# Performance work log

Hardware: AMD Instinct MI355X
Metric: run time of the kernel (lower is better)

## Reference

```python
import jax, jax.numpy as jnp
import numpy as np

BATCH, VOCAB = 256, 50257

def setup_inputs() -> dict:
    key = jax.random.key(0)
    k1, k2 = jax.random.split(key)
    logits = jax.random.normal(k1, (BATCH, VOCAB), dtype=jnp.float32) * 4.0  # LM-like logit spread
    temperature = jax.random.uniform(k2, (), dtype=jnp.float32, minval=0.5, maxval=1.5)
    return {"logits": logits, "temperature": temperature, "top_k": 50}


def reference(logits, temperature, top_k):
    # temperature scale (dividing by 1.0 is identical to the torch skip-branch)
    scaled = logits / temperature
    # top-k mask: keep exactly the k selected positions, -inf elsewhere
    top_vals, top_idx = jax.lax.top_k(scaled, top_k)          # [B, k]
    b = jnp.arange(scaled.shape[0])[:, None]                  # [B, 1]
    masked = jnp.full_like(scaled, -jnp.inf).at[b, top_idx].set(top_vals)
    # softmax + multinomial(num_samples=1) == categorical over masked logits
    key = jax.random.key(42)
    sampled = jax.random.categorical(key, masked, axis=-1)    # [B]
    return sampled
```

## Files before the change

kernel.cpp:

```cpp
#include <hip/hip_runtime.h>
#include <stdint.h>


#define VOCAB 50257
#define BATCH 256
#define NT 1024
#define NBINS 4096
#define CAND_CAP 2048
#define FILTER_VAL 4.0f
#define SPEC_VAL 10.0f

__device__ __forceinline__ uint32_t rotl32(uint32_t v, int r) {
  return (v << r) | (v >> (32 - r));
}

__device__ __forceinline__ void threefry2x32_42(uint32_t& x0, uint32_t& x1) {
  const uint32_t ks0 = 0u;
  const uint32_t ks1 = 42u;
  const uint32_t ks2 = ks0 ^ ks1 ^ 0x1BD11BDAu;
  x0 += ks0; x1 += ks1;
#define TF_R(r) { x0 += x1; x1 = rotl32(x1, (r)); x1 ^= x0; }
  TF_R(13) TF_R(15) TF_R(26) TF_R(6)
  x0 += ks1; x1 += ks2 + 1u;
  TF_R(17) TF_R(29) TF_R(16) TF_R(24)
  x0 += ks2; x1 += ks0 + 2u;
  TF_R(13) TF_R(15) TF_R(26) TF_R(6)
  x0 += ks0; x1 += ks1 + 3u;
  TF_R(17) TF_R(29) TF_R(16) TF_R(24)
  x0 += ks1; x1 += ks2 + 4u;
  TF_R(13) TF_R(15) TF_R(26) TF_R(6)
  x0 += ks2; x1 += ks0 + 5u;
#undef TF_R
}

__device__ __forceinline__ float gumbel_at(uint32_t flat) {
  uint32_t x0 = 0u, x1 = flat;
  threefry2x32_42(x0, x1);
  uint32_t bits = x0 ^ x1;
  uint32_t fb = (bits >> 9) | 0x3f800000u;
  float f = __uint_as_float(fb) - 1.0f;
  float u = fmaxf(f, 1.17549435e-38f);
  float t = (float)log((double)u);
  float g = (float)(-log((double)(-t)));
  return g;
}

__device__ __forceinline__ uint32_t fkey(float x) {
  uint32_t u = __float_as_uint(x);
  return (u & 0x80000000u) ? ~u : (u | 0x80000000u);
}

extern "C" __global__ void __launch_bounds__(NT)
topk_sample_kernel(const float* __restrict__ logits,
                   const float* __restrict__ temp_p,
                   const int* __restrict__ topk_p,
                   int* __restrict__ out) {
  const int row = blockIdx.x;
  const int tid = threadIdx.x;
  const float temp = temp_p[0];
  const int K = topk_p[0];
  const float* rowp = logits + (size_t)row * VOCAB;

  const int pc = (4 - (row & 3)) & 3;
  const int nv4 = (VOCAB - pc) >> 2;
  const int tailbase = pc + (nv4 << 2);
  const int tailc = VOCAB - tailbase;
  const float4* body = (const float4*)(rowp + pc);

  __shared__ unsigned hist[NBINS];
  __shared__ unsigned wtot[16];
  __shared__ unsigned aboveWave[16];
  __shared__ int sh_tb, sh_total, sh_cnt, sh_ok;
  __shared__ unsigned ckey[CAND_CAP];
  __shared__ int cidx[CAND_CAP];
  __shared__ float wbv[16];
  __shared__ int wbi[16];

  const int lane = tid & 63;
  const int wave = tid >> 6;

  float bestv = -__builtin_huge_valf();
  int besti = 0x7fffffff;
  bool done = false;

  if (tid == 0) { sh_cnt = 0; sh_ok = 0; }
  __syncthreads();
  if (tid < pc) {
    if (rowp[tid] >= SPEC_VAL) {
      int p = atomicAdd(&sh_cnt, 1);
      if (p < CAND_CAP) cidx[p] = tid;
    }
  }
  int v = tid;
  for (; v + 3 * NT < nv4; v += 4 * NT) {
    float4 x0 = body[v];
    float4 x1 = body[v + NT];
    float4 x2 = body[v + 2 * NT];
    float4 x3 = body[v + 3 * NT];
#define PROC4(VX, b)                                                             \
    {                                                                            \
      int base_ = (b);                                                           \
      if (VX.x >= SPEC_VAL) { int p = atomicAdd(&sh_cnt, 1); if (p < CAND_CAP) cidx[p] = base_; }     \
      if (VX.y >= SPEC_VAL) { int p = atomicAdd(&sh_cnt, 1); if (p < CAND_CAP) cidx[p] = base_ + 1; } \
      if (VX.z >= SPEC_VAL) { int p = atomicAdd(&sh_cnt, 1); if (p < CAND_CAP) cidx[p] = base_ + 2; } \
      if (VX.w >= SPEC_VAL) { int p = atomicAdd(&sh_cnt, 1); if (p < CAND_CAP) cidx[p] = base_ + 3; } \
    }
    PROC4(x0, pc + (v << 2))
    PROC4(x1, pc + ((v + NT) << 2))
    PROC4(x2, pc + ((v + 2 * NT) << 2))
    PROC4(x3, pc + ((v + 3 * NT) << 2))
  }
  for (; v < nv4; v += NT) {
    float4 x = body[v];
    PROC4(x, pc + (v << 2))
  }
#undef PROC4
  if (tid < tailc) {
    if (rowp[tailbase + tid] >= SPEC_VAL) {
      int p = atomicAdd(&sh_cnt, 1);
      if (p < CAND_CAP) cidx[p] = tailbase + tid;
    }
  }
  __syncthreads();
  const int total = sh_cnt;

  if (total >= K && total <= CAND_CAP) {
    const int C = total;
    float s_mine = 0.0f;
    if (tid < C) {
      s_mine = rowp[cidx[tid]] / temp;
      ckey[tid] = fkey(s_mine);
    }
    __syncthreads();
    if (tid < C) {
      const uint32_t mk = ckey[tid];
      const int mi = cidx[tid];
      int rank = 0;
      for (int j = 0; j < C; ++j) {
        uint32_t k = ckey[j];
        rank += (k > mk || (k == mk && cidx[j] < mi)) ? 1 : 0;
      }
      if (rank == K - 1) {
        sh_ok = (mk > fkey(SPEC_VAL / temp)) ? 1 : 0;
      }
      if (rank < K) {
        float v2 = s_mine + gumbel_at((uint32_t)row * (uint32_t)VOCAB + (uint32_t)mi);
        bestv = v2; besti = mi;
      }
    }
    __syncthreads();
    if (sh_ok) {
      done = true;
    } else {
      bestv = -__builtin_huge_valf();
      besti = 0x7fffffff;
    }
  }

  if (!done) {
    uint32_t filt = fkey(FILTER_VAL);
    int tb = 0;
    for (;;) {
      for (int b = tid; b < NBINS; b += NT) hist[b] = 0u;
      __syncthreads();
      if (tid < pc) {
        uint32_t k = fkey(rowp[tid]);
        if (k >= filt) atomicAdd(&hist[k >> 20], 1u);
      }
      for (int w = tid; w < nv4; w += NT) {
        float4 x = body[w];
        uint32_t k0 = fkey(x.x), k1 = fkey(x.y), k2 = fkey(x.z), k3 = fkey(x.w);
        if (k0 >= filt) atomicAdd(&hist[k0 >> 20], 1u);
        if (k1 >= filt) atomicAdd(&hist[k1 >> 20], 1u);
        if (k2 >= filt) atomicAdd(&hist[k2 >> 20], 1u);
        if (k3 >= filt) atomicAdd(&hist[k3 >> 20], 1u);
      }
      if (tid < tailc) {
        uint32_t k = fkey(rowp[tailbase + tid]);
        if (k >= filt) atomicAdd(&hist[k >> 20], 1u);
      }
      __syncthreads();

      unsigned p = hist[4 * tid] + hist[4 * tid + 1] + hist[4 * tid + 2] + hist[4 * tid + 3];
      unsigned vv = p;
      for (int off = 1; off < 64; off <<= 1) {
        unsigned o = (unsigned)__shfl_down((int)vv, off);
        if (lane + off < 64) vv += o;
      }
      if (lane == 0) wtot[wave] = vv;
      __syncthreads();
      if (tid == 0) {
        unsigned acc = 0;
        for (int w = 15; w >= 0; --w) { aboveWave[w] = acc; acc += wtot[w]; }
        sh_total = (int)acc;
      }
      __syncthreads();
      unsigned above = aboveWave[wave] + (vv - p);
      if (above < (unsigned)K && above + p >= (unsigned)K) {
        int need = K - (int)above;
        for (int b = 3; b >= 0; --b) {
          unsigned c = hist[4 * tid + b];
          if (c >= (unsigned)need) { sh_tb = 4 * tid + b; break; }
          need -= (int)c;
        }
      }
      __syncthreads();
      if (sh_total >= K) { tb = sh_tb; break; }
      filt = 0u;
      __syncthreads();
    }

    const uint32_t cutk = (uint32_t)max(tb - 1, 0) << 20;
    if (tid == 0) sh_cnt = 0;
    __syncthreads();
    if (tid < pc) {
      if (fkey(rowp[tid]) >= cutk) {
        int p = atomicAdd(&sh_cnt, 1);
        if (p < CAND_CAP) cidx[p] = tid;
      }
    }
    for (int w = tid; w < nv4; w += NT) {
      float4 x = body[w];
      int base = pc + (w << 2);
      if (fkey(x.x) >= cutk) { int p = atomicAdd(&sh_cnt, 1); if (p < CAND_CAP) cidx[p] = base; }
      if (fkey(x.y) >= cutk) { int p = atomicAdd(&sh_cnt, 1); if (p < CAND_CAP) cidx[p] = base + 1; }
      if (fkey(x.z) >= cutk) { int p = atomicAdd(&sh_cnt, 1); if (p < CAND_CAP) cidx[p] = base + 2; }
      if (fkey(x.w) >= cutk) { int p = atomicAdd(&sh_cnt, 1); if (p < CAND_CAP) cidx[p] = base + 3; }
    }
    if (tid < tailc) {
      if (fkey(rowp[tailbase + tid]) >= cutk) {
        int p = atomicAdd(&sh_cnt, 1);
        if (p < CAND_CAP) cidx[p] = tailbase + tid;
      }
    }
    __syncthreads();
    const int C = min(sh_cnt, CAND_CAP);

    if (tid < C) {
      int idx = cidx[tid];
      float s = rowp[idx] / temp;
      ckey[tid] = fkey(s);
    }
    __syncthreads();

    if (tid < C) {
      const uint32_t mk = ckey[tid];
      const int mi = cidx[tid];
      int rank = 0;
      for (int j = 0; j < C; ++j) {
        uint32_t k = ckey[j];
        rank += (k > mk || (k == mk && cidx[j] < mi)) ? 1 : 0;
      }
      if (rank < K) {
        float s = rowp[mi] / temp;
        float v2 = s + gumbel_at((uint32_t)row * (uint32_t)VOCAB + (uint32_t)mi);
        bestv = v2; besti = mi;
      }
    }
    __syncthreads();
  }

  for (int off = 32; off > 0; off >>= 1) {
    float v2 = __shfl_down(bestv, off);
    int i2 = __shfl_down(besti, off);
    if (v2 > bestv || (v2 == bestv && i2 < besti)) { bestv = v2; besti = i2; }
  }
  if (lane == 0) { wbv[wave] = bestv; wbi[wave] = besti; }
  __syncthreads();
  if (tid == 0) {
    float bv = wbv[0];
    int bi = wbi[0];
    for (int w = 1; w < 16; ++w) {
      float v2 = wbv[w];
      int i2 = wbi[w];
      if (v2 > bv || (v2 == bv && i2 < bi)) { bv = v2; bi = i2; }
    }
    out[row] = bi;
  }
}

extern "C" void kernel_launch(void* const* d_in, const int* in_sizes, int n_in,
                              void* d_out, int out_size, void* d_ws, size_t ws_size,
                              hipStream_t stream) {
  const float* logits = (const float*)d_in[0];
  const float* temp_p = (const float*)d_in[1];
  const int* topk_p = (const int*)d_in[2];
  int* out = (int*)d_out;
  hipLaunchKernelGGL(topk_sample_kernel, dim3(BATCH), dim3(NT), 0, stream,
                     logits, temp_p, topk_p, out);
}
```

Before: 114.5 us.

## Split row filtering across segment blocks and add separate refine/fallback kernels

The single kernel, which used one 1024-thread block per row, becomes three kernels. A filter kernel runs 16 segment blocks per row, each collecting indices of logits at or above the speculative threshold into a per-segment workspace slot. A refine kernel gathers the segments, ranks the candidates, samples with Gumbel noise, and sets a per-row flag. A fallback kernel, which exits early for flagged rows, runs the histogram path for the rest. This spreads the bandwidth-bound scan over many more blocks and CUs, but adds two extra kernel launches, workspace traffic, and a per-segment cap of 64 candidates that sends overflowing rows to the fallback path.

```diff
diff --git a/kernel.cpp b/kernel.cpp
--- a/kernel.cpp
+++ b/kernel.cpp
@@ -5,6 +5,10 @@
 #define VOCAB 50257
 #define BATCH 256
 #define NT 1024
+#define NTF 256
+#define NSEG 16
+#define SEG4 786
+#define CAP_SEG 64
 #define NBINS 4096
 #define CAND_CAP 2048
 #define FILTER_VAL 4.0f
@@ -50,15 +54,14 @@
   return (u & 0x80000000u) ? ~u : (u | 0x80000000u);
 }
 
-extern "C" __global__ void __launch_bounds__(NT)
-topk_sample_kernel(const float* __restrict__ logits,
-                   const float* __restrict__ temp_p,
-                   const int* __restrict__ topk_p,
-                   int* __restrict__ out) {
-  const int row = blockIdx.x;
+extern "C" __global__ void __launch_bounds__(NTF)
+filter_kernel(const float* __restrict__ logits,
+              int* __restrict__ cnt,
+              int* __restrict__ cand) {
+  const int b = blockIdx.x;
+  const int row = b >> 4;
+  const int seg = b & 15;
   const int tid = threadIdx.x;
-  const float temp = temp_p[0];
-  const int K = topk_p[0];
   const float* rowp = logits + (size_t)row * VOCAB;
 
   const int pc = (4 - (row & 3)) & 3;
@@ -67,10 +70,153 @@
   const int tailc = VOCAB - tailbase;
   const float4* body = (const float4*)(rowp + pc);
 
+  __shared__ int lcnt;
+  if (tid == 0) lcnt = 0;
+  __syncthreads();
+
+  int* myc = cand + (b << 6);
+  const int st = seg * SEG4;
+  const int en = min(nv4, st + SEG4);
+  for (int v = st + tid; v < en; v += NTF) {
+    float4 x = body[v];
+    int base = pc + (v << 2);
+    if (x.x >= SPEC_VAL) { int p = atomicAdd(&lcnt, 1); if (p < CAP_SEG) myc[p] = base; }
+    if (x.y >= SPEC_VAL) { int p = atomicAdd(&lcnt, 1); if (p < CAP_SEG) myc[p] = base + 1; }
+    if (x.z >= SPEC_VAL) { int p = atomicAdd(&lcnt, 1); if (p < CAP_SEG) myc[p] = base + 2; }
+    if (x.w >= SPEC_VAL) { int p = atomicAdd(&lcnt, 1); if (p < CAP_SEG) myc[p] = base + 3; }
+  }
+  if (seg == 0 && tid < pc) {
+    if (rowp[tid] >= SPEC_VAL) { int p = atomicAdd(&lcnt, 1); if (p < CAP_SEG) myc[p] = tid; }
+  }
+  if (seg == NSEG - 1 && tid < tailc) {
+    if (rowp[tailbase + tid] >= SPEC_VAL) {
+      int p = atomicAdd(&lcnt, 1); if (p < CAP_SEG) myc[p] = tailbase + tid;
+    }
+  }
+  __syncthreads();
+  if (tid == 0) cnt[b] = lcnt;
+}
+
+extern "C" __global__ void __launch_bounds__(NTF)
+refine_kernel(const float* __restrict__ logits,
+              const float* __restrict__ temp_p,
+              const int* __restrict__ topk_p,
+              int* __restrict__ out,
+              const int* __restrict__ cnt,
+              const int* __restrict__ cand,
+              int* __restrict__ flags) {
+  const int row = blockIdx.x;
+  const int tid = threadIdx.x;
+  const int lane = tid & 63;
+  const int wave = tid >> 6;
+
+  __shared__ int scnt[NSEG], soff[NSEG];
+  __shared__ int sh_total, sh_ok;
+  __shared__ unsigned ckey[CAND_CAP];
+  __shared__ int cidx[CAND_CAP];
+  __shared__ float wbv[4];
+  __shared__ int wbi[4];
+
+  if (tid < NSEG) scnt[tid] = cnt[(row << 4) + tid];
+  if (tid == 0) sh_ok = 0;
+  __syncthreads();
+  if (tid == 0) {
+    int acc = 0; int ovf = 0;
+    for (int s = 0; s < NSEG; ++s) {
+      soff[s] = acc;
+      if (scnt[s] > CAP_SEG) ovf = 1;
+      acc += scnt[s];
+    }
+    sh_total = ovf ? -1 : acc;
+  }
+  __syncthreads();
+  const int total = sh_total;
+  const int K = topk_p[0];
+  const float temp = temp_p[0];
+
+  const bool ok_path = (total >= K && total <= CAND_CAP);
+  if (ok_path) {
+    {
+      int s = tid >> 4, j0 = tid & 15;
+      const int* src = cand + (((row << 4) + s) << 6);
+      for (int j = j0; j < scnt[s]; j += 16) cidx[soff[s] + j] = src[j];
+    }
+    __syncthreads();
+    const float* rowp = logits + (size_t)row * VOCAB;
+    for (int c = tid; c < total; c += NTF) {
+      ckey[c] = fkey(rowp[cidx[c]] / temp);
+    }
+    __syncthreads();
+
+    float bestv = -__builtin_huge_valf();
+    int besti = 0x7fffffff;
+    const uint32_t cutkey = fkey(SPEC_VAL / temp);
+    for (int c = tid; c < total; c += NTF) {
+      const uint32_t mk = ckey[c];
+      const int mi = cidx[c];
+      int rank = 0;
+      for (int j = 0; j < total; ++j) {
+        uint32_t k = ckey[j];
+        rank += (k > mk || (k == mk && cidx[j] < mi)) ? 1 : 0;
+      }
+      if (rank == K - 1) {
+        sh_ok = (mk > cutkey) ? 1 : 0;
+      }
+      if (rank < K) {
+        float s = rowp[mi] / temp;
+        float v = s + gumbel_at((uint32_t)row * (uint32_t)VOCAB + (uint32_t)mi);
+        if (v > bestv || (v == bestv && mi < besti)) { bestv = v; besti = mi; }
+      }
+    }
+    __syncthreads();
+    if (sh_ok) {
+      for (int off = 32; off > 0; off >>= 1) {
+        float v2 = __shfl_down(bestv, off);
+        int i2 = __shfl_down(besti, off);
+        if (v2 > bestv || (v2 == bestv && i2 < besti)) { bestv = v2; besti = i2; }
+      }
+      if (lane == 0) { wbv[wave] = bestv; wbi[wave] = besti; }
+      __syncthreads();
+      if (tid == 0) {
+        float bv = wbv[0]; int bi = wbi[0];
+        for (int w = 1; w < 4; ++w) {
+          if (wbv[w] > bv || (wbv[w] == bv && wbi[w] < bi)) { bv = wbv[w]; bi = wbi[w]; }
+        }
+        out[row] = bi;
+        flags[row] = 1;
+      }
+    } else if (tid == 0) {
+      flags[row] = 0;
+    }
+  } else if (tid == 0) {
+    flags[row] = 0;
+  }
+}
+
+extern "C" __global__ void __launch_bounds__(NT)
+fallback_kernel(const float* __restrict__ logits,
+                const float* __restrict__ temp_p,
+                const int* __restrict__ topk_p,
+                int* __restrict__ out,
+                const int* __restrict__ flags) {
+  const int row = blockIdx.x;
+  if (flags[row]) return;
+
+  const int tid = threadIdx.x;
+  const float temp = temp_p[0];
+  const int K = topk_p[0];
+  const float* rowp = logits + (size_t)row * VOCAB;
+
+  const int pc = (4 - (row & 3)) & 3;
+  const int nv4 = (VOCAB - pc) >> 2;
+  const int tailbase = pc + (nv4 << 2);
+  const int tailc = VOCAB - tailbase;
+  const float4* body = (const float4*)(rowp + pc);
+
   __shared__ unsigned hist[NBINS];
   __shared__ unsigned wtot[16];
   __shared__ unsigned aboveWave[16];
-  __shared__ int sh_tb, sh_total, sh_cnt, sh_ok;
+  __shared__ int sh_tb, sh_total, sh_cnt;
   __shared__ unsigned ckey[CAND_CAP];
   __shared__ int cidx[CAND_CAP];
   __shared__ float wbv[16];
@@ -81,184 +227,107 @@
 
   float bestv = -__builtin_huge_valf();
   int besti = 0x7fffffff;
-  bool done = false;
-
-  if (tid == 0) { sh_cnt = 0; sh_ok = 0; }
+
+  uint32_t filt = fkey(FILTER_VAL);
+  int tb = 0;
+  for (;;) {
+    for (int b = tid; b < NBINS; b += NT) hist[b] = 0u;
+    __syncthreads();
+    if (tid < pc) {
+      uint32_t k = fkey(rowp[tid]);
+      if (k >= filt) atomicAdd(&hist[k >> 20], 1u);
+    }
+    for (int w = tid; w < nv4; w += NT) {
+      float4 x = body[w];
+      uint32_t k0 = fkey(x.x), k1 = fkey(x.y), k2 = fkey(x.z), k3 = fkey(x.w);
+      if (k0 >= filt) atomicAdd(&hist[k0 >> 20], 1u);
+      if (k1 >= filt) atomicAdd(&hist[k1 >> 20], 1u);
+      if (k2 >= filt) atomicAdd(&hist[k2 >> 20], 1u);
+      if (k3 >= filt) atomicAdd(&hist[k3 >> 20], 1u);
+    }
+    if (tid < tailc) {
+      uint32_t k = fkey(rowp[tailbase + tid]);
+      if (k >= filt) atomicAdd(&hist[k >> 20], 1u);
+    }
+    __syncthreads();
+
+    unsigned p = hist[4 * tid] + hist[4 * tid + 1] + hist[4 * tid + 2] + hist[4 * tid + 3];
+    unsigned vv = p;
+    for (int off = 1; off < 64; off <<= 1) {
+      unsigned o = (unsigned)__shfl_down((int)vv, off);
+      if (lane + off < 64) vv += o;
+    }
+    if (lane == 0) wtot[wave] = vv;
+    __syncthreads();
+    if (tid == 0) {
+      unsigned acc = 0;
+      for (int w = 15; w >= 0; --w) { aboveWave[w] = acc; acc += wtot[w]; }
+      sh_total = (int)acc;
+    }
+    __syncthreads();
+    unsigned above = aboveWave[wave] + (vv - p);
+    if (above < (unsigned)K && above + p >= (unsigned)K) {
+      int need = K - (int)above;
+      for (int b = 3; b >= 0; --b) {
+        unsigned c = hist[4 * tid + b];
+        if (c >= (unsigned)need) { sh_tb = 4 * tid + b; break; }
+        need -= (int)c;
+      }
+    }
+    __syncthreads();
+    if (sh_total >= K) { tb = sh_tb; break; }
+    filt = 0u;
+    __syncthreads();
+  }
+
+  const uint32_t cutk = (uint32_t)max(tb - 1, 0) << 20;
+  if (tid == 0) sh_cnt = 0;
   __syncthreads();
   if (tid < pc) {
-    if (rowp[tid] >= SPEC_VAL) {
+    if (fkey(rowp[tid]) >= cutk) {
       int p = atomicAdd(&sh_cnt, 1);
       if (p < CAND_CAP) cidx[p] = tid;
     }
   }
-  int v = tid;
-  for (; v + 3 * NT < nv4; v += 4 * NT) {
-    float4 x0 = body[v];
-    float4 x1 = body[v + NT];
-    float4 x2 = body[v + 2 * NT];
-    float4 x3 = body[v + 3 * NT];
-#define PROC4(VX, b)                                                             \
-    {                                                                            \
-      int base_ = (b);                                                           \
-      if (VX.x >= SPEC_VAL) { int p = atomicAdd(&sh_cnt, 1); if (p < CAND_CAP) cidx[p] = base_; }     \
-      if (VX.y >= SPEC_VAL) { int p = atomicAdd(&sh_cnt, 1); if (p < CAND_CAP) cidx[p] = base_ + 1; } \
-      if (VX.z >= SPEC_VAL) { int p = atomicAdd(&sh_cnt, 1); if (p < CAND_CAP) cidx[p] = base_ + 2; } \
-      if (VX.w >= SPEC_VAL) { int p = atomicAdd(&sh_cnt, 1); if (p < CAND_CAP) cidx[p] = base_ + 3; } \
-    }
-    PROC4(x0, pc + (v << 2))
-    PROC4(x1, pc + ((v + NT) << 2))
-    PROC4(x2, pc + ((v + 2 * NT) << 2))
-    PROC4(x3, pc + ((v + 3 * NT) << 2))
-  }
-  for (; v < nv4; v += NT) {
-    float4 x = body[v];
-    PROC4(x, pc + (v << 2))
-  }
-#undef PROC4
+  for (int w = tid; w < nv4; w += NT) {
+    float4 x = body[w];
+    int base = pc + (w << 2);
+    if (fkey(x.x) >= cutk) { int p = atomicAdd(&sh_cnt, 1); if (p < CAND_CAP) cidx[p] = base; }
+    if (fkey(x.y) >= cutk) { int p = atomicAdd(&sh_cnt, 1); if (p < CAND_CAP) cidx[p] = base + 1; }
+    if (fkey(x.z) >= cutk) { int p = atomicAdd(&sh_cnt, 1); if (p < CAND_CAP) cidx[p] = base + 2; }
+    if (fkey(x.w) >= cutk) { int p = atomicAdd(&sh_cnt, 1); if (p < CAND_CAP) cidx[p] = base + 3; }
+  }
   if (tid < tailc) {
-    if (rowp[tailbase + tid] >= SPEC_VAL) {
+    if (fkey(rowp[tailbase + tid]) >= cutk) {
       int p = atomicAdd(&sh_cnt, 1);
       if (p < CAND_CAP) cidx[p] = tailbase + tid;
     }
   }
   __syncthreads();
-  const int total = sh_cnt;
-
-  if (total >= K && total <= CAND_CAP) {
-    const int C = total;
-    float s_mine = 0.0f;
-    if (tid < C) {
-      s_mine = rowp[cidx[tid]] / temp;
-      ckey[tid] = fkey(s_mine);
-    }
-    __syncthreads();
-    if (tid < C) {
-      const uint32_t mk = ckey[tid];
-      const int mi = cidx[tid];
-      int rank = 0;
-      for (int j = 0; j < C; ++j) {
-        uint32_t k = ckey[j];
-        rank += (k > mk || (k == mk && cidx[j] < mi)) ? 1 : 0;
-      }
-      if (rank == K - 1) {
-        sh_ok = (mk > fkey(SPEC_VAL / temp)) ? 1 : 0;
-      }
-      if (rank < K) {
-        float v2 = s_mine + gumbel_at((uint32_t)row * (uint32_t)VOCAB + (uint32_t)mi);
-        bestv = v2; besti = mi;
-      }
-    }
-    __syncthreads();
-    if (sh_ok) {
-      done = true;
-    } else {
-      bestv = -__builtin_huge_valf();
-      besti = 0x7fffffff;
-    }
-  }
-
-  if (!done) {
-    uint32_t filt = fkey(FILTER_VAL);
-    int tb = 0;
-    for (;;) {
-      for (int b = tid; b < NBINS; b += NT) hist[b] = 0u;
-      __syncthreads();
-      if (tid < pc) {
-        uint32_t k = fkey(rowp[tid]);
-        if (k >= filt) atomicAdd(&hist[k >> 20], 1u);
-      }
-      for (int w = tid; w < nv4; w += NT) {
-        float4 x = body[w];
-        uint32_t k0 = fkey(x.x), k1 = fkey(x.y), k2 = fkey(x.z), k3 = fkey(x.w);
-        if (k0 >= filt) atomicAdd(&hist[k0 >> 20], 1u);
-        if (k1 >= filt) atomicAdd(&hist[k1 >> 20], 1u);
-        if (k2 >= filt) atomicAdd(&hist[k2 >> 20], 1u);
-        if (k3 >= filt) atomicAdd(&hist[k3 >> 20], 1u);
-      }
-      if (tid < tailc) {
-        uint32_t k = fkey(rowp[tailbase + tid]);
-        if (k >= filt) atomicAdd(&hist[k >> 20], 1u);
-      }
-      __syncthreads();
-
-      unsigned p = hist[4 * tid] + hist[4 * tid + 1] + hist[4 * tid + 2] + hist[4 * tid + 3];
-      unsigned vv = p;
-      for (int off = 1; off < 64; off <<= 1) {
-        unsigned o = (unsigned)__shfl_down((int)vv, off);
-        if (lane + off < 64) vv += o;
-      }
-      if (lane == 0) wtot[wave] = vv;
-      __syncthreads();
-      if (tid == 0) {
-        unsigned acc = 0;
-        for (int w = 15; w >= 0; --w) { aboveWave[w] = acc; acc += wtot[w]; }
-        sh_total = (int)acc;
-      }
-      __syncthreads();
-      unsigned above = aboveWave[wave] + (vv - p);
-      if (above < (unsigned)K && above + p >= (unsigned)K) {
-        int need = K - (int)above;
-        for (int b = 3; b >= 0; --b) {
-          unsigned c = hist[4 * tid + b];
-          if (c >= (unsigned)need) { sh_tb = 4 * tid + b; break; }
-          need -= (int)c;
-        }
-      }
-      __syncthreads();
-      if (sh_total >= K) { tb = sh_tb; break; }
-      filt = 0u;
-      __syncthreads();
-    }
-
-    const uint32_t cutk = (uint32_t)max(tb - 1, 0) << 20;
-    if (tid == 0) sh_cnt = 0;
-    __syncthreads();
-    if (tid < pc) {
-      if (fkey(rowp[tid]) >= cutk) {
-        int p = atomicAdd(&sh_cnt, 1);
-        if (p < CAND_CAP) cidx[p] = tid;
-      }
-    }
-    for (int w = tid; w < nv4; w += NT) {
-      float4 x = body[w];
-      int base = pc + (w << 2);
-      if (fkey(x.x) >= cutk) { int p = atomicAdd(&sh_cnt, 1); if (p < CAND_CAP) cidx[p] = base; }
-      if (fkey(x.y) >= cutk) { int p = atomicAdd(&sh_cnt, 1); if (p < CAND_CAP) cidx[p] = base + 1; }
-      if (fkey(x.z) >= cutk) { int p = atomicAdd(&sh_cnt, 1); if (p < CAND_CAP) cidx[p] = base + 2; }
-      if (fkey(x.w) >= cutk) { int p = atomicAdd(&sh_cnt, 1); if (p < CAND_CAP) cidx[p] = base + 3; }
-    }
-    if (tid < tailc) {
-      if (fkey(rowp[tailbase + tid]) >= cutk) {
-        int p = atomicAdd(&sh_cnt, 1);
-        if (p < CAND_CAP) cidx[p] = tailbase + tid;
-      }
-    }
-    __syncthreads();
-    const int C = min(sh_cnt, CAND_CAP);
-
-    if (tid < C) {
-      int idx = cidx[tid];
-      float s = rowp[idx] / temp;
-      ckey[tid] = fkey(s);
-    }
-    __syncthreads();
-
-    if (tid < C) {
-      const uint32_t mk = ckey[tid];
-      const int mi = cidx[tid];
-      int rank = 0;
-      for (int j = 0; j < C; ++j) {
-        uint32_t k = ckey[j];
-        rank += (k > mk || (k == mk && cidx[j] < mi)) ? 1 : 0;
-      }
-      if (rank < K) {
-        float s = rowp[mi] / temp;
-        float v2 = s + gumbel_at((uint32_t)row * (uint32_t)VOCAB + (uint32_t)mi);
-        bestv = v2; besti = mi;
-      }
-    }
-    __syncthreads();
-  }
+  const int C = min(sh_cnt, CAND_CAP);
+
+  if (tid < C) {
+    int idx = cidx[tid];
+    float s = rowp[idx] / temp;
+    ckey[tid] = fkey(s);
+  }
+  __syncthreads();
+
+  if (tid < C) {
+    const uint32_t mk = ckey[tid];
+    const int mi = cidx[tid];
+    int rank = 0;
+    for (int j = 0; j < C; ++j) {
+      uint32_t k = ckey[j];
+      rank += (k > mk || (k == mk && cidx[j] < mi)) ? 1 : 0;
+    }
+    if (rank < K) {
+      float s = rowp[mi] / temp;
+      float v2 = s + gumbel_at((uint32_t)row * (uint32_t)VOCAB + (uint32_t)mi);
+      bestv = v2; besti = mi;
+    }
+  }
+  __syncthreads();
 
   for (int off = 32; off > 0; off >>= 1) {
     float v2 = __shfl_down(bestv, off);
@@ -271,9 +340,7 @@
     float bv = wbv[0];
     int bi = wbi[0];
     for (int w = 1; w < 16; ++w) {
-      float v2 = wbv[w];
-      int i2 = wbi[w];
-      if (v2 > bv || (v2 == bv && i2 < bi)) { bv = v2; bi = i2; }
+      if (wbv[w] > bv || (wbv[w] == bv && wbi[w] < bi)) { bv = wbv[w]; bi = wbi[w]; }
     }
     out[row] = bi;
   }
@@ -286,6 +353,15 @@
   const float* temp_p = (const float*)d_in[1];
   const int* topk_p = (const int*)d_in[2];
   int* out = (int*)d_out;
-  hipLaunchKernelGGL(topk_sample_kernel, dim3(BATCH), dim3(NT), 0, stream,
-                     logits, temp_p, topk_p, out);
-}
+
+  int* cnt = (int*)d_ws;
+  int* cand = cnt + BATCH * NSEG;
+  int* flags = cand + BATCH * NSEG * CAP_SEG;
+
+  hipLaunchKernelGGL(filter_kernel, dim3(BATCH * NSEG), dim3(NTF), 0, stream,
+                     logits, cnt, cand);
+  hipLaunchKernelGGL(refine_kernel, dim3(BATCH), dim3(NTF), 0, stream,
+                     logits, temp_p, topk_p, out, cnt, cand, flags);
+  hipLaunchKernelGGL(fallback_kernel, dim3(BATCH), dim3(NT), 0, stream,
+                     logits, temp_p, topk_p, out, flags);
+}
```

Result: slower. 147.1 us (+28.5%).
